# Optimization experiments

Hardware: AMD Instinct MI355X
Metric: run time of the kernel (lower is better)

Reference implementation:

```python
import jax, jax.numpy as jnp
import numpy as np
from jax import lax

DIM = 128
DEPTH = 2
OUT_DIM = 256
DIM_HEAD = 64
HEADS = 8
WS = 16
INNER = DIM_HEAD * HEADS
EPS = 1e-5
SCALE = DIM_HEAD ** (-0.5)


def setup_inputs() -> dict:
    key = jax.random.key(0)
    ks = jax.random.split(key, 20)
    s = 0.02
    L = DEPTH
    inp = {
        "x": jax.random.normal(ks[0], (1, DIM, 256, 256), dtype=jnp.float32),
        "ln1_g": jnp.ones((L, DIM), dtype=jnp.float32),
        "ln1_b": jnp.zeros((L, DIM), dtype=jnp.float32),
        "wq": jax.random.normal(ks[1], (L, INNER, DIM), dtype=jnp.float32) * s,
        "wkv": jax.random.normal(ks[2], (L, 2 * INNER, DIM), dtype=jnp.float32) * s,
        "wo": jax.random.normal(ks[3], (L, DIM, INNER), dtype=jnp.float32) * s,
        "bo": jnp.zeros((L, DIM), dtype=jnp.float32),
        "ln2_g": jnp.ones((L, DIM), dtype=jnp.float32),
        "ln2_b": jnp.zeros((L, DIM), dtype=jnp.float32),
        "w_in": jax.random.normal(ks[4], (L, DIM, DIM), dtype=jnp.float32) * s,
        "b_in": jnp.zeros((L, DIM), dtype=jnp.float32),
        "w_c3": jax.random.normal(ks[5], (L, OUT_DIM, DIM, 3, 3), dtype=jnp.float32) * s,
        "b_c3": jnp.zeros((L, OUT_DIM), dtype=jnp.float32),
        "w_c1": jax.random.normal(ks[6], (L, DIM, OUT_DIM), dtype=jnp.float32) * s,
        "b_c1": jnp.zeros((L, DIM), dtype=jnp.float32),
        "w_outer": jax.random.normal(ks[7], (DIM, DIM), dtype=jnp.float32) * s,
        "b_outer": jnp.zeros((DIM,), dtype=jnp.float32),
    }
    return inp


def _layernorm(x, g, b):
    # channel-wise (dim=1) norm; note torch code uses (std + eps), not sqrt(var + eps)
    mean = jnp.mean(x, axis=1, keepdims=True)
    std = jnp.sqrt(jnp.var(x, axis=1, keepdims=True))
    return (x - mean) / (std + EPS) * g[None, :, None, None] + b[None, :, None, None]


def _conv1x1(w, x, b=None):
    y = jnp.einsum('oi,bihw->bohw', w, x)
    if b is not None:
        y = y + b[None, :, None, None]
    return y


def _to_windows(t, B, H, W):
    # [B, HEADS*DIM_HEAD, H, W] -> [B*HEADS*nx*ny, WS*WS, DIM_HEAD]
    nx, ny = H // WS, W // WS
    t = t.reshape(B, HEADS, DIM_HEAD, nx, WS, ny, WS)
    t = t.transpose(0, 1, 3, 5, 4, 6, 2)
    return t.reshape(B * HEADS * nx * ny, WS * WS, DIM_HEAD)


def _from_windows(t, B, H, W):
    nx, ny = H // WS, W // WS
    t = t.reshape(B, HEADS, nx, ny, WS, WS, DIM_HEAD)
    t = t.transpose(0, 1, 6, 2, 4, 3, 5)
    return t.reshape(B, HEADS * DIM_HEAD, H, W)


def _attention(x, wq_l, wkv_l, wo_l, bo_l):
    B, _, H, W = x.shape
    q = _conv1x1(wq_l, x)
    kv = _conv1x1(wkv_l, x)
    k, v = kv[:, :INNER], kv[:, INNER:]
    q = _to_windows(q, B, H, W)
    k = _to_windows(k, B, H, W)
    v = _to_windows(v, B, H, W)
    sim = jnp.einsum('bid,bjd->bij', q, k) * SCALE  # [nwin, 256, 256]
    attn = jax.nn.softmax(sim, axis=-1)
    out = jnp.einsum('bij,bjd->bid', attn, v)
    out = _from_windows(out, B, H, W)
    return _conv1x1(wo_l, out, bo_l)


def _feedforward(x, w_in_l, b_in_l, w_c3_l, b_c3_l, w_c1_l, b_c1_l):
    h = _conv1x1(w_in_l, x, b_in_l)
    h = lax.conv_general_dilated(h, w_c3_l, window_strides=(1, 1), padding='SAME',
                                 dimension_numbers=('NCHW', 'OIHW', 'NCHW'))
    h = h + b_c3_l[None, :, None, None]
    h = jax.nn.gelu(h, approximate=False)
    return _conv1x1(w_c1_l, h, b_c1_l)


def reference(x, ln1_g, ln1_b, wq, wkv, wo, bo, ln2_g, ln2_b,
              w_in, b_in, w_c3, b_c3, w_c1, b_c1, w_outer, b_outer):
    for l in range(DEPTH):
        xn = _layernorm(x, ln1_g[l], ln1_b[l])
        x = _attention(xn, wq[l], wkv[l], wo[l], bo[l]) + x
        xn = _layernorm(x, ln2_g[l], ln2_b[l])
        x = _feedforward(xn, w_in[l], b_in[l], w_c3[l], b_c3[l], w_c1[l], b_c1[l]) + x
    return _conv1x1(w_outer, x, b_outer) + x
```

## Files before the change

kernel.cpp:

```cpp
#include <hip/hip_runtime.h>
#include <hip/hip_bf16.h>
#include <math.h>

typedef __hip_bfloat16 bf16;
typedef float f4 __attribute__((ext_vector_type(4)));
typedef short s8 __attribute__((ext_vector_type(8)));
typedef unsigned int u2 __attribute__((ext_vector_type(2)));
typedef unsigned int u4v __attribute__((ext_vector_type(4)));

__device__ __forceinline__ void gload16(const void* g, char* l) {
  __builtin_amdgcn_global_load_lds(
      (const __attribute__((address_space(1))) unsigned int*)g,
      (__attribute__((address_space(3))) unsigned int*)l, 16, 0, 0);
}
__device__ __forceinline__ unsigned short bfr(float f) {
  bf16 h = __float2bfloat16(f);
  return *(unsigned short*)&h;
}
__device__ __forceinline__ unsigned int pk2(float a, float b) {
  return (unsigned int)bfr(a) | ((unsigned int)bfr(b) << 16);
}
__device__ __forceinline__ unsigned int pkt(float a, float b) {
  return __builtin_amdgcn_perm(__float_as_uint(b), __float_as_uint(a), 0x07060302u);
}

__global__ __launch_bounds__(256) void prep_w(
    const float* __restrict__ wq, const float* __restrict__ wkv,
    const float* __restrict__ wo, const float* __restrict__ win,
    const float* __restrict__ wc3, const float* __restrict__ wc1,
    const float* __restrict__ wout, ushort* __restrict__ cw)
{
  int i = blockIdx.x * 256 + threadIdx.x;
  float v;
  if (i < 131072) v = wq[i];
  else if (i < 393216) v = wkv[i - 131072];
  else if (i < 524288) v = wo[i - 393216];
  else if (i < 557056) v = win[i - 524288];
  else if (i < 1146880) {
    int j = i - 557056; int lyr = j / 294912; int r = j - lyr * 294912;
    int m = r / 1152; int k = r - m * 1152; int tap = k >> 7; int ic = k & 127;
    v = wc3[(((size_t)lyr * 256 + m) * 128 + ic) * 9 + tap];
  }
  else if (i < 1212416) v = wc1[i - 1146880];
  else if (i < 1228800) v = wout[i - 1212416];
  else if (i < 1230848) { cw[i] = 0; return; }
  else return;
  cw[i] = bfr(v);
}

template<bool NCHW>
__global__ __launch_bounds__(256) void ln_nhwc(
    const float* __restrict__ x, const float* __restrict__ g,
    const float* __restrict__ b, ushort* __restrict__ y)
{
  const int p = blockIdx.x * 256 + threadIdx.x;
  f4 v[32];
  float s = 0.f, s2 = 0.f;
  if constexpr (NCHW) {
#pragma unroll
    for (int i = 0; i < 32; ++i)
#pragma unroll
      for (int j = 0; j < 4; ++j) {
        float t = x[(size_t)(i * 4 + j) * 65536 + p];
        v[i][j] = t; s += t; s2 += t * t;
      }
  } else {
    const f4* base = (const f4*)(x + (size_t)p * 128);
#pragma unroll
    for (int i = 0; i < 32; ++i) {
      v[i] = base[i];
#pragma unroll
      for (int j = 0; j < 4; ++j) { s += v[i][j]; s2 += v[i][j] * v[i][j]; }
    }
  }
  float mean = s * (1.f / 128.f);
  float var = s2 * (1.f / 128.f) - mean * mean;
  var = var > 0.f ? var : 0.f;
  float inv = 1.f / (sqrtf(var) + 1e-5f);
  u2* dst = (u2*)(y + (size_t)p * 128);
#pragma unroll
  for (int i = 0; i < 32; ++i) {
    f4 gg = *(const f4*)(g + i * 4);
    f4 bb = *(const f4*)(b + i * 4);
    float f0 = (v[i][0] - mean) * inv * gg[0] + bb[0];
    float f1 = (v[i][1] - mean) * inv * gg[1] + bb[1];
    float f2 = (v[i][2] - mean) * inv * gg[2] + bb[2];
    float f3 = (v[i][3] - mean) * inv * gg[3] + bb[3];
    u2 st; st.x = pk2(f0, f1); st.y = pk2(f2, f3);
    dst[i] = st;
  }
}

template<int MODE>
__global__ __launch_bounds__(256) void gemm_nhwc(
    const ushort* __restrict__ A, const ushort* __restrict__ X,
    const float* __restrict__ bias, const float* __restrict__ res,
    void* __restrict__ out, ushort* __restrict__ out2, const int K, const int M)
{
  __shared__ __align__(16) char sm[32768];
  const int tid = threadIdx.x, w = tid >> 6, l = tid & 63;
  const int quad = l >> 4, l15 = l & 15;
  const int n0 = blockIdx.x * 128, m0 = blockIdx.y * 128;
  const int mh = (w & 1) * 64, nh = (w >> 1) * 64;
  const f4 fz = {0.f, 0.f, 0.f, 0.f};
  f4 acc[4][4];
#pragma unroll
  for (int a = 0; a < 4; ++a)
#pragma unroll
    for (int b2 = 0; b2 < 4; ++b2) acc[a][b2] = fz;

  const int KI = K >> 6;
  for (int kk = 0; kk < KI; ++kk) {
    if (kk) __syncthreads();
    const int k0 = kk << 6;
#pragma unroll
    for (int j = 0; j < 4; ++j) {
      int p = j * 256 + tid, r = p >> 3, c = (p & 7) ^ (r & 7);
      gload16(A + (size_t)(m0 + r) * K + k0 + c * 8, sm + (j * 256 + w * 64) * 16);
    }
#pragma unroll
    for (int j = 0; j < 4; ++j) {
      int p = j * 256 + tid, r = p >> 3, c = (p & 7) ^ (r & 7);
      gload16(X + (size_t)(n0 + r) * K + k0 + c * 8, sm + 16384 + (j * 256 + w * 64) * 16);
    }
    __syncthreads();
#pragma unroll
    for (int ks = 0; ks < 2; ++ks) {
      s8 af[4], bx[4];
#pragma unroll
      for (int mt = 0; mt < 4; ++mt) {
        int rr = mh + mt * 16 + l15;
        af[mt] = *(const s8*)(sm + rr * 128 + (((ks * 4 + quad) ^ (rr & 7)) << 4));
      }
#pragma unroll
      for (int nt = 0; nt < 4; ++nt) {
        int rr = nh + nt * 16 + l15;
        bx[nt] = *(const s8*)(sm + 16384 + rr * 128 + (((ks * 4 + quad) ^ (rr & 7)) << 4));
      }
#pragma unroll
      for (int mt = 0; mt < 4; ++mt)
#pragma unroll
        for (int nt = 0; nt < 4; ++nt)
          acc[mt][nt] = __builtin_amdgcn_mfma_f32_16x16x32_bf16(af[mt], bx[nt], acc[mt][nt], 0, 0, 0);
    }
  }
#pragma unroll
  for (int mt = 0; mt < 4; ++mt) {
#pragma unroll
    for (int nt = 0; nt < 4; ++nt) {
      const int m = m0 + mh + mt * 16 + quad * 4;
      const int n = n0 + nh + nt * 16 + l15;
      f4 bb = *(const f4*)(bias + m);
      f4 v = acc[mt][nt] + bb;
      if constexpr (MODE == 0) {
        u2 st; st.x = pk2(v[0], v[1]); st.y = pk2(v[2], v[3]);
        *(u2*)((ushort*)out + (size_t)n * M + m) = st;
      } else if constexpr (MODE == 1 || MODE == 3) {
        f4 r = *(const f4*)(res + (size_t)n * M + m);
        v += r;
        *(f4*)((float*)out + (size_t)n * M + m) = v;
        if constexpr (MODE == 3) {
          u2 st; st.x = pk2(v[0], v[1]); st.y = pk2(v[2], v[3]);
          *(u2*)(out2 + (size_t)n * M + m) = st;
        }
      } else if constexpr (MODE == 4) {
        f4 r;
#pragma unroll
        for (int i = 0; i < 4; ++i) r[i] = res[(size_t)(m + i) * 65536 + n];
        v += r;
        *(f4*)((float*)out + (size_t)n * M + m) = v;
      } else {
        f4 r = *(const f4*)(res + (size_t)n * M + m);
#pragma unroll
        for (int i = 0; i < 4; ++i)
          ((float*)out)[(size_t)(m + i) * 65536 + n] = v[i] + r[i];
      }
    }
  }
}

__global__ __launch_bounds__(256) void conv3_kernel(
    const ushort* __restrict__ A, const ushort* __restrict__ X,
    const float* __restrict__ bias, ushort* __restrict__ out,
    const ushort* __restrict__ zp)
{
  __shared__ __align__(16) char sm[32768];
  const int tid = threadIdx.x, w = tid >> 6, l = tid & 63;
  const int quad = l >> 4, l15 = l & 15;
  const int n0 = blockIdx.x * 128, m0 = blockIdx.y * 128;
  const int mh = (w & 1) * 64, nh = (w >> 1) * 64;
  const f4 fz = {0.f, 0.f, 0.f, 0.f};
  f4 acc[4][4];
#pragma unroll
  for (int a = 0; a < 4; ++a)
#pragma unroll
    for (int b2 = 0; b2 < 4; ++b2) acc[a][b2] = fz;

  for (int kk = 0; kk < 18; ++kk) {
    if (kk) __syncthreads();
    const int tap = kk >> 1, ky = tap / 3, kx = tap - ky * 3;
    const int dn = (ky - 1) * 256 + (kx - 1);
    const int kseg = (kk & 1) << 6;
#pragma unroll
    for (int j = 0; j < 4; ++j) {
      int p = j * 256 + tid, r = p >> 3, c = (p & 7) ^ (r & 7);
      gload16(A + (size_t)(m0 + r) * 1152 + kk * 64 + c * 8, sm + (j * 256 + w * 64) * 16);
    }
#pragma unroll
    for (int j = 0; j < 4; ++j) {
      int p = j * 256 + tid, r = p >> 3, c = (p & 7) ^ (r & 7);
      int nl = n0 + r;
      int ys = (nl >> 8) + ky - 1, xs = (nl & 255) + kx - 1;
      const ushort* gp = ((unsigned)ys < 256u && (unsigned)xs < 256u)
                         ? X + (size_t)(nl + dn) * 128 + kseg + c * 8 : zp;
      gload16(gp, sm + 16384 + (j * 256 + w * 64) * 16);
    }
    __syncthreads();
#pragma unroll
    for (int ks = 0; ks < 2; ++ks) {
      s8 af[4], bx[4];
#pragma unroll
      for (int mt = 0; mt < 4; ++mt) {
        int rr = mh + mt * 16 + l15;
        af[mt] = *(const s8*)(sm + rr * 128 + (((ks * 4 + quad) ^ (rr & 7)) << 4));
      }
#pragma unroll
      for (int nt = 0; nt < 4; ++nt) {
        int rr = nh + nt * 16 + l15;
        bx[nt] = *(const s8*)(sm + 16384 + rr * 128 + (((ks * 4 + quad) ^ (rr & 7)) << 4));
      }
#pragma unroll
      for (int mt = 0; mt < 4; ++mt)
#pragma unroll
        for (int nt = 0; nt < 4; ++nt)
          acc[mt][nt] = __builtin_amdgcn_mfma_f32_16x16x32_bf16(af[mt], bx[nt], acc[mt][nt], 0, 0, 0);
    }
  }
#pragma unroll
  for (int mt = 0; mt < 4; ++mt) {
#pragma unroll
    for (int nt = 0; nt < 4; ++nt) {
      const int m = m0 + mh + mt * 16 + quad * 4;
      const int n = n0 + nh + nt * 16 + l15;
      f4 bb = *(const f4*)(bias + m);
      f4 v = acc[mt][nt] + bb;
      float g0 = 0.5f * v[0] * (1.f + erff(v[0] * 0.70710678118f));
      float g1 = 0.5f * v[1] * (1.f + erff(v[1] * 0.70710678118f));
      float g2 = 0.5f * v[2] * (1.f + erff(v[2] * 0.70710678118f));
      float g3 = 0.5f * v[3] * (1.f + erff(v[3] * 0.70710678118f));
      u2 st; st.x = pk2(g0, g1); st.y = pk2(g2, g3);
      *(u2*)(out + (size_t)n * 256 + m) = st;
    }
  }
}

__global__ __launch_bounds__(512) void attn_kernel(
    const ushort* __restrict__ xn, const ushort* __restrict__ wq,
    const ushort* __restrict__ wkv, ushort* __restrict__ ao)
{
  __shared__ __align__(16) char sm[147456];
  const int tid = threadIdx.x, w = tid >> 6, l = tid & 63;
  const int quad = l >> 4, l15 = l & 15;
  const int win = blockIdx.x, head = blockIdx.y;
  const int nbase = ((win >> 4) << 12) + ((win & 15) << 4);
  char* RX  = sm;
  char* RW  = sm + 65536;
  char* RK  = sm + 114688;
  char* RVT = sm;
  char* Pw  = sm + 32768 + w * 4096;
  char* RO  = RW;
  const f4 fz = {0.f, 0.f, 0.f, 0.f};

#pragma unroll
  for (int j = 0; j < 8; ++j) {
    int p = j * 512 + tid, r = p >> 4, c = (p & 15) ^ (r & 15);
    int n = nbase + ((r >> 4) << 8) + (r & 15);
    gload16(xn + (size_t)n * 128 + c * 8, RX + (j * 512 + w * 64) * 16);
  }
  {
    const ushort* wpq = wq + (size_t)head * 64 * 128;
    const ushort* wpk = wkv + (size_t)head * 64 * 128;
    const ushort* wpv = wkv + (size_t)(512 + head * 64) * 128;
#pragma unroll
    for (int j = 0; j < 2; ++j) {
      int p = j * 512 + tid, r = p >> 4, c = (p & 15) ^ (r & 15);
      gload16(wpq + (size_t)r * 128 + c * 8, RW + (j * 512 + w * 64) * 16);
    }
#pragma unroll
    for (int j = 0; j < 2; ++j) {
      int p = j * 512 + tid, r = p >> 4, c = (p & 15) ^ (r & 15);
      gload16(wpk + (size_t)r * 128 + c * 8, RW + 16384 + (j * 512 + w * 64) * 16);
    }
#pragma unroll
    for (int j = 0; j < 2; ++j) {
      int p = j * 512 + tid, r = p >> 4, c = (p & 15) ^ (r & 15);
      gload16(wpv + (size_t)r * 128 + c * 8, RW + 32768 + (j * 512 + w * 64) * 16);
    }
  }
  __syncthreads();

  s8 bq[2][2];
  {
    f4 acc[4][2];
#pragma unroll
    for (int a = 0; a < 4; ++a) { acc[a][0] = fz; acc[a][1] = fz; }
#pragma unroll
    for (int ks = 0; ks < 4; ++ks) {
      s8 af[4], bx[2];
#pragma unroll
      for (int mt = 0; mt < 4; ++mt) {
        int rr = mt * 16 + l15;
        af[mt] = *(const s8*)(RW + rr * 256 + (((ks * 4 + quad) ^ (rr & 15)) << 4));
      }
#pragma unroll
      for (int nt = 0; nt < 2; ++nt) {
        int rr = w * 32 + nt * 16 + l15;
        bx[nt] = *(const s8*)(RX + rr * 256 + (((ks * 4 + quad) ^ (rr & 15)) << 4));
      }
#pragma unroll
      for (int mt = 0; mt < 4; ++mt)
#pragma unroll
        for (int nt = 0; nt < 2; ++nt)
          acc[mt][nt] = __builtin_amdgcn_mfma_f32_16x16x32_bf16(af[mt], bx[nt], acc[mt][nt], 0, 0, 0);
    }
#pragma unroll
    for (int nt = 0; nt < 2; ++nt) {
      unsigned pd[4][2];
#pragma unroll
      for (int mt = 0; mt < 4; ++mt) {
        pd[mt][0] = pkt(acc[mt][nt][0], acc[mt][nt][1]);
        pd[mt][1] = pkt(acc[mt][nt][2], acc[mt][nt][3]);
      }
#pragma unroll
      for (int ks = 0; ks < 2; ++ks) {
        u4v t;
#pragma unroll
        for (int dj = 0; dj < 4; ++dj) {
          int srcl = l15 + (((quad & 1) * 2 + (dj >> 1)) << 4);
          unsigned va = (unsigned)__shfl((int)pd[2 * ks][dj & 1], srcl, 64);
          unsigned vb = (unsigned)__shfl((int)pd[2 * ks + 1][dj & 1], srcl, 64);
          t[dj] = (quad < 2) ? va : vb;
        }
        bq[nt][ks] = __builtin_bit_cast(s8, t);
      }
    }
  }

  {
    f4 acc[4][2];
#pragma unroll
    for (int a = 0; a < 4; ++a) { acc[a][0] = fz; acc[a][1] = fz; }
#pragma unroll
    for (int ks = 0; ks < 4; ++ks) {
      s8 af[4], bx[2];
#pragma unroll
      for (int mt = 0; mt < 4; ++mt) {
        int rr = mt * 16 + l15;
        af[mt] = *(const s8*)(RW + 16384 + rr * 256 + (((ks * 4 + quad) ^ (rr & 15)) << 4));
      }
#pragma unroll
      for (int nt = 0; nt < 2; ++nt) {
        int rr = w * 32 + nt * 16 + l15;
        bx[nt] = *(const s8*)(RX + rr * 256 + (((ks * 4 + quad) ^ (rr & 15)) << 4));
      }
#pragma unroll
      for (int mt = 0; mt < 4; ++mt)
#pragma unroll
        for (int nt = 0; nt < 2; ++nt)
          acc[mt][nt] = __builtin_amdgcn_mfma_f32_16x16x32_bf16(af[mt], bx[nt], acc[mt][nt], 0, 0, 0);
    }
#pragma unroll
    for (int mt = 0; mt < 4; ++mt)
#pragma unroll
      for (int nt = 0; nt < 2; ++nt) {
        int tok = w * 32 + nt * 16 + l15, d0 = mt * 16 + quad * 4;
        char* a = RK + tok * 128 + (((d0 >> 3) ^ (tok & 7)) << 4) + (d0 & 7) * 2;
        *(unsigned int*)a = pkt(acc[mt][nt][0], acc[mt][nt][1]);
        *(unsigned int*)(a + 4) = pkt(acc[mt][nt][2], acc[mt][nt][3]);
      }
  }

  {
    f4 acc[2][4];
#pragma unroll
    for (int a = 0; a < 2; ++a)
#pragma unroll
      for (int b2 = 0; b2 < 4; ++b2) acc[a][b2] = fz;
#pragma unroll
    for (int ks = 0; ks < 4; ++ks) {
      s8 ax[2], bw[4];
#pragma unroll
      for (int mt = 0; mt < 2; ++mt) {
        int rr = w * 32 + mt * 16 + l15;
        ax[mt] = *(const s8*)(RX + rr * 256 + (((ks * 4 + quad) ^ (rr & 15)) << 4));
      }
#pragma unroll
      for (int nt = 0; nt < 4; ++nt) {
        int rr = nt * 16 + l15;
        bw[nt] = *(const s8*)(RW + 32768 + rr * 256 + (((ks * 4 + quad) ^ (rr & 15)) << 4));
      }
#pragma unroll
      for (int mt = 0; mt < 2; ++mt)
#pragma unroll
        for (int nt = 0; nt < 4; ++nt)
          acc[mt][nt] = __builtin_amdgcn_mfma_f32_16x16x32_bf16(ax[mt], bw[nt], acc[mt][nt], 0, 0, 0);
    }
    __syncthreads();
#pragma unroll
    for (int mt = 0; mt < 2; ++mt)
#pragma unroll
      for (int nt = 0; nt < 4; ++nt) {
        int d = nt * 16 + l15, t0 = w * 32 + mt * 16 + quad * 4;
        char* a = RVT + d * 512 + (((t0 >> 3) ^ (d & 31)) << 4) + (t0 & 7) * 2;
        *(unsigned int*)a = pkt(acc[mt][nt][0], acc[mt][nt][1]);
        *(unsigned int*)(a + 4) = pkt(acc[mt][nt][2], acc[mt][nt][3]);
      }
  }
  __syncthreads();

  f4 o[4][2];
  float lsum[2] = {0.f, 0.f};
#pragma unroll
  for (int a = 0; a < 4; ++a) { o[a][0] = fz; o[a][1] = fz; }

  for (int jt = 0; jt < 4; ++jt) {
    f4 s[4][2];
#pragma unroll
    for (int a = 0; a < 4; ++a) { s[a][0] = fz; s[a][1] = fz; }
#pragma unroll
    for (int ks = 0; ks < 2; ++ks) {
      s8 af[4];
#pragma unroll
      for (int mt = 0; mt < 4; ++mt) {
        int rr = jt * 64 + mt * 16 + l15;
        af[mt] = *(const s8*)(RK + rr * 128 + (((ks * 4 + quad) ^ (rr & 7)) << 4));
      }
#pragma unroll
      for (int mt = 0; mt < 4; ++mt)
#pragma unroll
        for (int nt = 0; nt < 2; ++nt)
          s[mt][nt] = __builtin_amdgcn_mfma_f32_16x16x32_bf16(af[mt], bq[nt][ks], s[mt][nt], 0, 0, 0);
    }
#pragma unroll
    for (int mt = 0; mt < 4; ++mt)
#pragma unroll
      for (int nt = 0; nt < 2; ++nt) {
        float p0 = exp2f(s[mt][nt][0] * 0.18033688f);
        float p1 = exp2f(s[mt][nt][1] * 0.18033688f);
        float p2 = exp2f(s[mt][nt][2] * 0.18033688f);
        float p3 = exp2f(s[mt][nt][3] * 0.18033688f);
        lsum[nt] += p0 + p1 + p2 + p3;
        int iL = nt * 16 + l15, j0 = mt * 16 + quad * 4;
        char* a = Pw + iL * 128 + (((j0 >> 3) ^ (iL & 7)) << 4) + (j0 & 7) * 2;
        *(unsigned int*)a = pkt(p0, p1);
        *(unsigned int*)(a + 4) = pkt(p2, p3);
      }
#pragma unroll
    for (int ks = 0; ks < 2; ++ks) {
      s8 av[4], bp[2];
#pragma unroll
      for (int mt = 0; mt < 4; ++mt) {
        int d = mt * 16 + l15;
        av[mt] = *(const s8*)(RVT + d * 512 + (((jt * 8 + ks * 4 + quad) ^ (d & 31)) << 4));
      }
#pragma unroll
      for (int nt = 0; nt < 2; ++nt) {
        int iL = nt * 16 + l15;
        bp[nt] = *(const s8*)(Pw + iL * 128 + (((ks * 4 + quad) ^ (iL & 7)) << 4));
      }
#pragma unroll
      for (int mt = 0; mt < 4; ++mt)
#pragma unroll
        for (int nt = 0; nt < 2; ++nt)
          o[mt][nt] = __builtin_amdgcn_mfma_f32_16x16x32_bf16(av[mt], bp[nt], o[mt][nt], 0, 0, 0);
    }
  }

  float inv[2];
#pragma unroll
  for (int nt = 0; nt < 2; ++nt) {
    float v = lsum[nt];
    v += __shfl_xor(v, 16, 64);
    v += __shfl_xor(v, 32, 64);
    inv[nt] = 1.f / v;
  }
#pragma unroll
  for (int mt = 0; mt < 4; ++mt)
#pragma unroll
    for (int nt = 0; nt < 2; ++nt) {
      int i = w * 32 + nt * 16 + l15, d0 = mt * 16 + quad * 4;
      char* a = RO + i * 128 + (((d0 >> 3) ^ (i & 7)) << 4) + (d0 & 7) * 2;
      *(unsigned int*)a = pkt(o[mt][nt][0] * inv[nt], o[mt][nt][1] * inv[nt]);
      *(unsigned int*)(a + 4) = pkt(o[mt][nt][2] * inv[nt], o[mt][nt][3] * inv[nt]);
    }
  __syncthreads();
  const int tok = tid >> 1, half = tid & 1;
  const int n = nbase + ((tok >> 4) << 8) + (tok & 15);
  ushort* dst = ao + (size_t)n * 512 + head * 64 + half * 32;
#pragma unroll
  for (int c = 0; c < 4; ++c) {
    u4v v = *(const u4v*)(RO + tok * 128 + (((half * 4 + c) ^ (tok & 7)) << 4));
    *(u4v*)(dst + c * 8) = v;
  }
}

extern "C" void kernel_launch(void* const* d_in, const int* in_sizes, int n_in,
                              void* d_out, int out_size, void* d_ws, size_t ws_size,
                              hipStream_t stream)
{
  const float* x_in    = (const float*)d_in[0];
  const float* ln1_g   = (const float*)d_in[1];
  const float* ln1_b   = (const float*)d_in[2];
  const float* wq      = (const float*)d_in[3];
  const float* wkv     = (const float*)d_in[4];
  const float* wo      = (const float*)d_in[5];
  const float* bo      = (const float*)d_in[6];
  const float* ln2_g   = (const float*)d_in[7];
  const float* ln2_b   = (const float*)d_in[8];
  const float* w_in    = (const float*)d_in[9];
  const float* b_in    = (const float*)d_in[10];
  const float* w_c3    = (const float*)d_in[11];
  const float* b_c3    = (const float*)d_in[12];
  const float* w_c1    = (const float*)d_in[13];
  const float* b_c1    = (const float*)d_in[14];
  const float* w_outer = (const float*)d_in[15];
  const float* b_outer = (const float*)d_in[16];

  char* wsb = (char*)d_ws;
  ushort* CW = (ushort*)wsb;
  float*  XH = (float*)(wsb + 4194304);
  ushort* XN = (ushort*)(wsb + 37748736);
  ushort* AO = (ushort*)(wsb + 54525952);
  ushort* H  = (ushort*)(wsb + 121634816);
  ushort* G  = (ushort*)(wsb + 138412032);
  ushort* XB = (ushort*)(wsb + 171966464);

  const ushort* zp = CW + 1228800;
  dim3 b256(256);

  prep_w<<<dim3(4808), b256, 0, stream>>>(wq, wkv, wo, w_in, w_c3, w_c1, w_outer, CW);

  for (int lyr = 0; lyr < 2; ++lyr) {
    const ushort* cwq = CW + lyr * 65536;
    const ushort* cwkv = CW + 131072 + lyr * 131072;
    const ushort* cwo = CW + 393216 + lyr * 65536;
    const ushort* cwin = CW + 524288 + lyr * 16384;
    const ushort* cw3 = CW + 557056 + lyr * 294912;
    const ushort* cwc1 = CW + 1146880 + lyr * 32768;

    if (lyr == 0)
      ln_nhwc<true><<<dim3(256), b256, 0, stream>>>(x_in, ln1_g, ln1_b, XN);
    else
      ln_nhwc<false><<<dim3(256), b256, 0, stream>>>(XH, ln1_g + lyr * 128, ln1_b + lyr * 128, XN);

    attn_kernel<<<dim3(256, 8), dim3(512), 0, stream>>>(XN, cwq, cwkv, AO);

    if (lyr == 0)
      gemm_nhwc<4><<<dim3(512, 1), b256, 0, stream>>>(cwo, AO, bo, x_in, XH, nullptr, 512, 128);
    else
      gemm_nhwc<1><<<dim3(512, 1), b256, 0, stream>>>(cwo, AO, bo + lyr * 128, XH, XH, nullptr, 512, 128);

    ln_nhwc<false><<<dim3(256), b256, 0, stream>>>(XH, ln2_g + lyr * 128, ln2_b + lyr * 128, XN);
    gemm_nhwc<0><<<dim3(512, 1), b256, 0, stream>>>(cwin, XN, b_in + lyr * 128, nullptr, H, nullptr, 128, 128);
    conv3_kernel<<<dim3(512, 2), b256, 0, stream>>>(cw3, H, b_c3 + lyr * 256, G, zp);

    if (lyr == 1)
      gemm_nhwc<3><<<dim3(512, 1), b256, 0, stream>>>(cwc1, G, b_c1 + lyr * 128, XH, XH, XB, 256, 128);
    else
      gemm_nhwc<1><<<dim3(512, 1), b256, 0, stream>>>(cwc1, G, b_c1 + lyr * 128, XH, XH, nullptr, 256, 128);
  }
  gemm_nhwc<2><<<dim3(512, 1), b256, 0, stream>>>(CW + 1212416, XB, b_outer, XH, d_out, nullptr, 128, 128);
}
```

Before: 655.7 us.

## Shrink attention kernel LDS by loading X and weights directly into registers

The attention kernel stops staging the window's input tokens and the per-head Q/K/V weight slices in shared memory. X fragments now go straight into registers and weight fragments are read from global memory inside each projection loop. The softmax probabilities are repacked into MFMA operands with cross-lane shuffles instead of a per-wave LDS scratch buffer. LDS use drops from 144 KB to 64 KB and launch bounds request more resident blocks, aiming for higher occupancy. The cost is repeated uncached global weight loads per wave, more register pressure, and an extra barrier before the output staging.

```diff
diff --git a/kernel.cpp b/kernel.cpp
--- a/kernel.cpp
+++ b/kernel.cpp
@@ -254,50 +254,33 @@
   }
 }
 
-__global__ __launch_bounds__(512) void attn_kernel(
+__global__ __launch_bounds__(512, 4) void attn_kernel(
     const ushort* __restrict__ xn, const ushort* __restrict__ wq,
     const ushort* __restrict__ wkv, ushort* __restrict__ ao)
 {
-  __shared__ __align__(16) char sm[147456];
+  __shared__ __align__(16) char sm[65536];
   const int tid = threadIdx.x, w = tid >> 6, l = tid & 63;
   const int quad = l >> 4, l15 = l & 15;
   const int win = blockIdx.x, head = blockIdx.y;
   const int nbase = ((win >> 4) << 12) + ((win & 15) << 4);
-  char* RX  = sm;
-  char* RW  = sm + 65536;
-  char* RK  = sm + 114688;
-  char* RVT = sm;
-  char* Pw  = sm + 32768 + w * 4096;
-  char* RO  = RW;
+  char* RK  = sm;
+  char* RVT = sm + 32768;
+  char* RO  = sm;
   const f4 fz = {0.f, 0.f, 0.f, 0.f};
 
-#pragma unroll
-  for (int j = 0; j < 8; ++j) {
-    int p = j * 512 + tid, r = p >> 4, c = (p & 15) ^ (r & 15);
-    int n = nbase + ((r >> 4) << 8) + (r & 15);
-    gload16(xn + (size_t)n * 128 + c * 8, RX + (j * 512 + w * 64) * 16);
-  }
-  {
-    const ushort* wpq = wq + (size_t)head * 64 * 128;
-    const ushort* wpk = wkv + (size_t)head * 64 * 128;
-    const ushort* wpv = wkv + (size_t)(512 + head * 64) * 128;
-#pragma unroll
-    for (int j = 0; j < 2; ++j) {
-      int p = j * 512 + tid, r = p >> 4, c = (p & 15) ^ (r & 15);
-      gload16(wpq + (size_t)r * 128 + c * 8, RW + (j * 512 + w * 64) * 16);
-    }
-#pragma unroll
-    for (int j = 0; j < 2; ++j) {
-      int p = j * 512 + tid, r = p >> 4, c = (p & 15) ^ (r & 15);
-      gload16(wpk + (size_t)r * 128 + c * 8, RW + 16384 + (j * 512 + w * 64) * 16);
-    }
-#pragma unroll
-    for (int j = 0; j < 2; ++j) {
-      int p = j * 512 + tid, r = p >> 4, c = (p & 15) ^ (r & 15);
-      gload16(wpv + (size_t)r * 128 + c * 8, RW + 32768 + (j * 512 + w * 64) * 16);
-    }
-  }
-  __syncthreads();
+  const ushort* wpq = wq + (size_t)head * 64 * 128;
+  const ushort* wpk = wkv + (size_t)head * 64 * 128;
+  const ushort* wpv = wkv + (size_t)(512 + head * 64) * 128;
+
+  const int xrow0 = (nbase + (w * 2 + 0) * 256 + l15) * 128;
+  const int xrow1 = (nbase + (w * 2 + 1) * 256 + l15) * 128;
+
+  s8 xf[2][4];
+#pragma unroll
+  for (int ks = 0; ks < 4; ++ks) {
+    xf[0][ks] = *(const s8*)(xn + xrow0 + (ks * 4 + quad) * 8);
+    xf[1][ks] = *(const s8*)(xn + xrow1 + (ks * 4 + quad) * 8);
+  }
 
   s8 bq[2][2];
   {
@@ -306,22 +289,15 @@
     for (int a = 0; a < 4; ++a) { acc[a][0] = fz; acc[a][1] = fz; }
 #pragma unroll
     for (int ks = 0; ks < 4; ++ks) {
-      s8 af[4], bx[2];
-#pragma unroll
-      for (int mt = 0; mt < 4; ++mt) {
-        int rr = mt * 16 + l15;
-        af[mt] = *(const s8*)(RW + rr * 256 + (((ks * 4 + quad) ^ (rr & 15)) << 4));
-      }
-#pragma unroll
-      for (int nt = 0; nt < 2; ++nt) {
-        int rr = w * 32 + nt * 16 + l15;
-        bx[nt] = *(const s8*)(RX + rr * 256 + (((ks * 4 + quad) ^ (rr & 15)) << 4));
-      }
+      s8 af[4];
+#pragma unroll
+      for (int mt = 0; mt < 4; ++mt)
+        af[mt] = *(const s8*)(wpq + (mt * 16 + l15) * 128 + (ks * 4 + quad) * 8);
 #pragma unroll
       for (int mt = 0; mt < 4; ++mt)
 #pragma unroll
         for (int nt = 0; nt < 2; ++nt)
-          acc[mt][nt] = __builtin_amdgcn_mfma_f32_16x16x32_bf16(af[mt], bx[nt], acc[mt][nt], 0, 0, 0);
+          acc[mt][nt] = __builtin_amdgcn_mfma_f32_16x16x32_bf16(af[mt], xf[nt][ks], acc[mt][nt], 0, 0, 0);
     }
 #pragma unroll
     for (int nt = 0; nt < 2; ++nt) {
@@ -352,22 +328,15 @@
     for (int a = 0; a < 4; ++a) { acc[a][0] = fz; acc[a][1] = fz; }
 #pragma unroll
     for (int ks = 0; ks < 4; ++ks) {
-      s8 af[4], bx[2];
-#pragma unroll
-      for (int mt = 0; mt < 4; ++mt) {
-        int rr = mt * 16 + l15;
-        af[mt] = *(const s8*)(RW + 16384 + rr * 256 + (((ks * 4 + quad) ^ (rr & 15)) << 4));
-      }
-#pragma unroll
-      for (int nt = 0; nt < 2; ++nt) {
-        int rr = w * 32 + nt * 16 + l15;
-        bx[nt] = *(const s8*)(RX + rr * 256 + (((ks * 4 + quad) ^ (rr & 15)) << 4));
-      }
+      s8 af[4];
+#pragma unroll
+      for (int mt = 0; mt < 4; ++mt)
+        af[mt] = *(const s8*)(wpk + (mt * 16 + l15) * 128 + (ks * 4 + quad) * 8);
 #pragma unroll
       for (int mt = 0; mt < 4; ++mt)
 #pragma unroll
         for (int nt = 0; nt < 2; ++nt)
-          acc[mt][nt] = __builtin_amdgcn_mfma_f32_16x16x32_bf16(af[mt], bx[nt], acc[mt][nt], 0, 0, 0);
+          acc[mt][nt] = __builtin_amdgcn_mfma_f32_16x16x32_bf16(af[mt], xf[nt][ks], acc[mt][nt], 0, 0, 0);
     }
 #pragma unroll
     for (int mt = 0; mt < 4; ++mt)
@@ -388,24 +357,16 @@
       for (int b2 = 0; b2 < 4; ++b2) acc[a][b2] = fz;
 #pragma unroll
     for (int ks = 0; ks < 4; ++ks) {
-      s8 ax[2], bw[4];
-#pragma unroll
-      for (int mt = 0; mt < 2; ++mt) {
-        int rr = w * 32 + mt * 16 + l15;
-        ax[mt] = *(const s8*)(RX + rr * 256 + (((ks * 4 + quad) ^ (rr & 15)) << 4));
-      }
-#pragma unroll
-      for (int nt = 0; nt < 4; ++nt) {
-        int rr = nt * 16 + l15;
-        bw[nt] = *(const s8*)(RW + 32768 + rr * 256 + (((ks * 4 + quad) ^ (rr & 15)) << 4));
-      }
+      s8 bw[4];
+#pragma unroll
+      for (int nt = 0; nt < 4; ++nt)
+        bw[nt] = *(const s8*)(wpv + (nt * 16 + l15) * 128 + (ks * 4 + quad) * 8);
 #pragma unroll
       for (int mt = 0; mt < 2; ++mt)
 #pragma unroll
         for (int nt = 0; nt < 4; ++nt)
-          acc[mt][nt] = __builtin_amdgcn_mfma_f32_16x16x32_bf16(ax[mt], bw[nt], acc[mt][nt], 0, 0, 0);
-    }
-    __syncthreads();
+          acc[mt][nt] = __builtin_amdgcn_mfma_f32_16x16x32_bf16(xf[mt][ks], bw[nt], acc[mt][nt], 0, 0, 0);
+    }
 #pragma unroll
     for (int mt = 0; mt < 2; ++mt)
 #pragma unroll
@@ -441,38 +402,46 @@
         for (int nt = 0; nt < 2; ++nt)
           s[mt][nt] = __builtin_amdgcn_mfma_f32_16x16x32_bf16(af[mt], bq[nt][ks], s[mt][nt], 0, 0, 0);
     }
-#pragma unroll
-    for (int mt = 0; mt < 4; ++mt)
-#pragma unroll
-      for (int nt = 0; nt < 2; ++nt) {
+    s8 bp[2][2];
+#pragma unroll
+    for (int nt = 0; nt < 2; ++nt) {
+      unsigned pd[4][2];
+#pragma unroll
+      for (int mt = 0; mt < 4; ++mt) {
         float p0 = exp2f(s[mt][nt][0] * 0.18033688f);
         float p1 = exp2f(s[mt][nt][1] * 0.18033688f);
         float p2 = exp2f(s[mt][nt][2] * 0.18033688f);
         float p3 = exp2f(s[mt][nt][3] * 0.18033688f);
         lsum[nt] += p0 + p1 + p2 + p3;
-        int iL = nt * 16 + l15, j0 = mt * 16 + quad * 4;
-        char* a = Pw + iL * 128 + (((j0 >> 3) ^ (iL & 7)) << 4) + (j0 & 7) * 2;
-        *(unsigned int*)a = pkt(p0, p1);
-        *(unsigned int*)(a + 4) = pkt(p2, p3);
-      }
+        pd[mt][0] = pkt(p0, p1);
+        pd[mt][1] = pkt(p2, p3);
+      }
+#pragma unroll
+      for (int ks = 0; ks < 2; ++ks) {
+        u4v t;
+#pragma unroll
+        for (int dj = 0; dj < 4; ++dj) {
+          int srcl = l15 + (((quad & 1) * 2 + (dj >> 1)) << 4);
+          unsigned va = (unsigned)__shfl((int)pd[2 * ks][dj & 1], srcl, 64);
+          unsigned vb = (unsigned)__shfl((int)pd[2 * ks + 1][dj & 1], srcl, 64);
+          t[dj] = (quad < 2) ? va : vb;
+        }
+        bp[nt][ks] = __builtin_bit_cast(s8, t);
+      }
+    }
 #pragma unroll
     for (int ks = 0; ks < 2; ++ks) {
-      s8 av[4], bp[2];
+      s8 av[4];
 #pragma unroll
       for (int mt = 0; mt < 4; ++mt) {
         int d = mt * 16 + l15;
         av[mt] = *(const s8*)(RVT + d * 512 + (((jt * 8 + ks * 4 + quad) ^ (d & 31)) << 4));
       }
 #pragma unroll
-      for (int nt = 0; nt < 2; ++nt) {
-        int iL = nt * 16 + l15;
-        bp[nt] = *(const s8*)(Pw + iL * 128 + (((ks * 4 + quad) ^ (iL & 7)) << 4));
-      }
-#pragma unroll
       for (int mt = 0; mt < 4; ++mt)
 #pragma unroll
         for (int nt = 0; nt < 2; ++nt)
-          o[mt][nt] = __builtin_amdgcn_mfma_f32_16x16x32_bf16(av[mt], bp[nt], o[mt][nt], 0, 0, 0);
+          o[mt][nt] = __builtin_amdgcn_mfma_f32_16x16x32_bf16(av[mt], bp[nt][ks], o[mt][nt], 0, 0, 0);
     }
   }
 
@@ -484,6 +453,7 @@
     v += __shfl_xor(v, 32, 64);
     inv[nt] = 1.f / v;
   }
+  __syncthreads();
 #pragma unroll
   for (int mt = 0; mt < 4; ++mt)
 #pragma unroll
```

New measurement: 729.6 us. 1.11x slower.
